# Kernel optimization log

Measured on AMD Instinct MI355X. Metric: run time of the kernel, lower is better.

## Reference

```python
import jax, jax.numpy as jnp
import numpy as np

N_NODES = 100000


def setup_inputs() -> dict:
    key = jax.random.key(0)
    ks = jax.random.split(key, 6)
    x = jax.random.normal(ks[0], (N_NODES, 128), dtype=jnp.float32)
    edge_index = jax.random.randint(ks[1], (2, 1600000), 0, N_NODES, dtype=jnp.int32)
    W_gcn = jax.random.normal(ks[2], (128, 128), dtype=jnp.float32) * 0.05
    b_gcn = jax.random.normal(ks[3], (128,), dtype=jnp.float32) * 0.05
    W_fc = jax.random.normal(ks[4], (64, 128), dtype=jnp.float32) * 0.05
    b_fc = jax.random.normal(ks[5], (64,), dtype=jnp.float32) * 0.05
    return {"x": x, "edge_index": edge_index, "W_gcn": W_gcn, "b_gcn": b_gcn, "W_fc": W_fc, "b_fc": b_fc}


def _gcn_conv(x, edge_index, W, b):
    N = x.shape[0]
    # add self-loops (PyG GCNConv default add_self_loops=True)
    loops = jnp.arange(N, dtype=edge_index.dtype)
    row = jnp.concatenate([edge_index[0], loops])  # source
    col = jnp.concatenate([edge_index[1], loops])  # target (aggregation index)
    # symmetric normalization: deg computed at target with unit edge weights
    deg = jax.ops.segment_sum(jnp.ones_like(col, dtype=x.dtype), col, num_segments=N)
    deg_inv_sqrt = jnp.where(deg > 0, jax.lax.rsqrt(deg), 0.0)
    norm = deg_inv_sqrt[row] * deg_inv_sqrt[col]  # [E+N]
    xw = x @ W  # [N, nhid] - transform before aggregation
    msgs = norm[:, None] * xw[row]  # gather + scale, [E+N, nhid]
    out = jax.ops.segment_sum(msgs, col, num_segments=N)  # scatter-add
    return out + b


def reference(x, edge_index, W_gcn, b_gcn, W_fc, b_fc):
    h = _gcn_conv(x, edge_index, W_gcn, b_gcn)  # [N, nhid]
    return h @ W_fc.T + b_fc  # [N, nclass]
```

## Files before the change

kernel.cpp:

```cpp
#include <hip/hip_runtime.h>
#include <hip/hip_bf16.h>

typedef __hip_bfloat16 bf16;

#define N_NODES 100000
#define N_EDGES 1600000
#define F_IN    128
#define F_OUT   64
#define NBLK    391

#define NB_BKT   196
#define BKT_SH   9
#define BKT_CAP  8960
#define LBIN_CAP 56
#define EPB_A    4096


typedef __attribute__((ext_vector_type(8))) short vbf8;
typedef __attribute__((ext_vector_type(4))) float vf4;

__device__ __forceinline__ float ldf(const void* p, size_t i, bool isbf) {
    return isbf ? __bfloat162float(((const bf16*)p)[i]) : ((const float*)p)[i];
}
__device__ __forceinline__ void stf(void* p, size_t i, bool isbf, float v) {
    if (isbf) ((bf16*)p)[i] = __float2bfloat16(v);
    else      ((float*)p)[i] = v;
}
__device__ __forceinline__ unsigned short f2bfu(float f) {
    __hip_bfloat16 h = __float2bfloat16(f);
    union { __hip_bfloat16 h; unsigned short u; } c; c.h = h; return c.u;
}
__device__ __forceinline__ float bflo(unsigned int u) { return __uint_as_float(u << 16); }
__device__ __forceinline__ float bfhi(unsigned int u) { return __uint_as_float(u & 0xffff0000u); }

__device__ __forceinline__ void splitbf(float f, short& h, short& l) {
    unsigned short hu = f2bfu(f);
    float hf = bflo((unsigned)hu << 0 ? (unsigned)hu << 16 >> 16 << 16 : 0u);
    (void)hf;
    h = (short)hu;
    l = (short)f2bfu(f - __uint_as_float((unsigned)hu << 16));
}

__global__ void k_detect(const unsigned short* __restrict__ w, int* __restrict__ flag) {
    int l = threadIdx.x;
    int good = 0;
#pragma unroll
    for (int q = 0; q < 2; ++q) {
        unsigned short v = w[2 * (l + 64 * q)];
        int e = (v >> 7) & 0xFF;
        if ((e >= 100 && e <= 140) || ((v & 0x7FFF) == 0)) good++;
    }
    unsigned long long m1 = __ballot(good >= 1), m2 = __ballot(good >= 2);
    if (l == 0) *flag = (__popcll(m1) + __popcll(m2) >= 96) ? 1 : 0;
}

__global__ void k_weights(const int* __restrict__ flag,
                          const void* __restrict__ Wg, const void* __restrict__ bg,
                          const void* __restrict__ Wf, const void* __restrict__ bfc,
                          float* __restrict__ M, float* __restrict__ cvec,
                          bf16* __restrict__ Mhi, bf16* __restrict__ Mlo) {
    bool isbf = (*flag != 0);
    int t = blockIdx.x * blockDim.x + threadIdx.x;
    if (t >= F_IN * F_OUT) return;
    int k = t >> 6, c = t & 63;
    float s = 0.f;
    for (int j = 0; j < F_IN; ++j)
        s += ldf(Wg, k * F_IN + j, isbf) * ldf(Wf, c * F_IN + j, isbf);
    M[k * F_OUT + c] = s;
    if (Mhi) {
        int l    = (((k >> 3) & 3) << 4) | (c & 15);
        int fidx = ((((k >> 5) << 2) + (c >> 4)) * 64 + l) * 8 + (k & 7);
        bf16 h  = __float2bfloat16(s);
        Mhi[fidx] = h;
        Mlo[fidx] = __float2bfloat16(s - __bfloat162float(h));
    }
    if (k == 0) {
        float cs = ldf(bfc, c, isbf);
        for (int j = 0; j < F_IN; ++j)
            cs += ldf(bg, j, isbf) * ldf(Wf, c * F_IN + j, isbf);
        cvec[c] = cs;
    }
}


__global__ void k_zero(int* __restrict__ gtail) {
    int i = threadIdx.x;
    if (i < NB_BKT) gtail[i] = 0;
}

__global__ __launch_bounds__(256) void k_binA(const int* __restrict__ ei,
                                              int* __restrict__ gtail,
                                              unsigned* __restrict__ bkt) {
    __shared__ unsigned lbin[NB_BKT * LBIN_CAP];
    __shared__ int lcnt[NB_BKT];
    __shared__ int lbase[NB_BKT];
    int t = threadIdx.x;
    for (int b = t; b < NB_BKT; b += 256) lcnt[b] = 0;
    __syncthreads();
    int e0 = blockIdx.x * EPB_A;
#pragma unroll
    for (int q = 0; q < EPB_A / 256; ++q) {
        int e = e0 + q * 256 + t;
        if (e < N_EDGES) {
            int r = ei[e], c = ei[N_EDGES + e];
            int b = c >> BKT_SH;
            unsigned val = (unsigned)r | ((unsigned)(c & ((1 << BKT_SH) - 1)) << 17);
            int p = atomicAdd(&lcnt[b], 1);
            if (p < LBIN_CAP) {
                lbin[b * LBIN_CAP + p] = val;
            } else {
                int gp = atomicAdd(&gtail[b], 1);
                if (gp < BKT_CAP) bkt[(size_t)b * BKT_CAP + gp] = val;
            }
        }
    }
    __syncthreads();
    for (int b = t; b < NB_BKT; b += 256) {
        int n = min(lcnt[b], LBIN_CAP);
        lbase[b] = atomicAdd(&gtail[b], n);
    }
    __syncthreads();
    int w = t >> 6, l = t & 63;
    for (int b = w; b < NB_BKT; b += 4) {
        int nB = min(lcnt[b], LBIN_CAP);
        int gp0 = lbase[b];
        for (int i = l; i < nB; i += 64) {
            int gp = gp0 + i;
            if (gp < BKT_CAP) bkt[(size_t)b * BKT_CAP + gp] = lbin[b * LBIN_CAP + i];
        }
    }
}

__global__ void k_bktscan(const int* __restrict__ gtail, int* __restrict__ bbase) {
    __shared__ int sm[256];
    int t = threadIdx.x;
    int v = (t < NB_BKT) ? min(gtail[t], BKT_CAP) : 0;
    sm[t] = v; __syncthreads();
    for (int s = 1; s < 256; s <<= 1) {
        int add = (t >= s) ? sm[t - s] : 0;
        __syncthreads();
        sm[t] += add;
        __syncthreads();
    }
    if (t < NB_BKT) bbase[t] = sm[t] - v;
}

__global__ __launch_bounds__(512) void k_build(const unsigned* __restrict__ bkt,
                                               const int* __restrict__ gtail,
                                               const int* __restrict__ bbase,
                                               int* __restrict__ ptr,
                                               int* __restrict__ cnt,
                                               float* __restrict__ dinv,
                                               int* __restrict__ srcs) {
    __shared__ int cntl[512], sm[512], fill[512];
    int b = blockIdx.x, t = threadIdx.x;
    int n = min(gtail[b], BKT_CAP);
    int base = bbase[b];
    cntl[t] = 0;
    __syncthreads();
    for (int i = t; i < n; i += 512)
        atomicAdd(&cntl[bkt[(size_t)b * BKT_CAP + i] >> 17], 1);
    __syncthreads();
    int v = cntl[t];
    sm[t] = v; __syncthreads();
    for (int s = 1; s < 512; s <<= 1) {
        int add = (t >= s) ? sm[t - s] : 0;
        __syncthreads();
        sm[t] += add;
        __syncthreads();
    }
    int excl = sm[t] - v;
    fill[t] = excl;
    int node = (b << BKT_SH) + t;
    if (node < N_NODES) {
        ptr[node]  = base + excl;
        cnt[node]  = v;
        dinv[node] = rsqrtf((float)(v + 1));
    }
    __syncthreads();
    for (int i = t; i < n; i += 512) {
        unsigned e = bkt[(size_t)b * BKT_CAP + i];
        int c = (int)(e >> 17);
        int p = atomicAdd(&fill[c], 1);
        srcs[base + p] = (int)(e & 0x1FFFF);
    }
}

__global__ __launch_bounds__(256) void k_xmz_mfma(const int* __restrict__ flag,
                                                  const void* __restrict__ x,
                                                  const bf16* __restrict__ Mhi,
                                                  const bf16* __restrict__ Mlo,
                                                  const float* __restrict__ dinv,
                                                  bf16* __restrict__ y) {
    int t = threadIdx.x;
    int w = t >> 6, lane = t & 63;
    int g = lane >> 4, cb = lane & 15;
    int r0 = blockIdx.x * 64 + w * 16;
    int rr = min(r0 + cb, N_NODES - 1);
    bool isbf = (*flag != 0);
    const vbf8* Bh = (const vbf8*)Mhi;
    const vbf8* Bl = (const vbf8*)Mlo;
    vf4 acc0 = {0.f,0.f,0.f,0.f}, acc1 = {0.f,0.f,0.f,0.f};
    vf4 acc2 = {0.f,0.f,0.f,0.f}, acc3 = {0.f,0.f,0.f,0.f};

    if (isbf) {
        const vbf8* X8 = (const vbf8*)x;
#pragma unroll
        for (int kk = 0; kk < 4; ++kk) {
            vbf8 a = X8[(size_t)rr * 16 + kk * 4 + g];
            int bb = kk * 256 + lane;
            acc0 = __builtin_amdgcn_mfma_f32_16x16x32_bf16(a, Bh[bb      ], acc0, 0, 0, 0);
            acc0 = __builtin_amdgcn_mfma_f32_16x16x32_bf16(a, Bl[bb      ], acc0, 0, 0, 0);
            acc1 = __builtin_amdgcn_mfma_f32_16x16x32_bf16(a, Bh[bb +  64], acc1, 0, 0, 0);
            acc1 = __builtin_amdgcn_mfma_f32_16x16x32_bf16(a, Bl[bb +  64], acc1, 0, 0, 0);
            acc2 = __builtin_amdgcn_mfma_f32_16x16x32_bf16(a, Bh[bb + 128], acc2, 0, 0, 0);
            acc2 = __builtin_amdgcn_mfma_f32_16x16x32_bf16(a, Bl[bb + 128], acc2, 0, 0, 0);
            acc3 = __builtin_amdgcn_mfma_f32_16x16x32_bf16(a, Bh[bb + 192], acc3, 0, 0, 0);
            acc3 = __builtin_amdgcn_mfma_f32_16x16x32_bf16(a, Bl[bb + 192], acc3, 0, 0, 0);
        }
    } else {
        const float4* X4 = (const float4*)x;
#pragma unroll
        for (int kk = 0; kk < 4; ++kk) {
            float4 v0 = X4[(size_t)rr * 32 + kk * 8 + g * 2];
            float4 v1 = X4[(size_t)rr * 32 + kk * 8 + g * 2 + 1];
            vbf8 ah, al;
            {
                float fv[8] = {v0.x, v0.y, v0.z, v0.w, v1.x, v1.y, v1.z, v1.w};
#pragma unroll
                for (int i = 0; i < 8; ++i) {
                    unsigned short hu = f2bfu(fv[i]);
                    ah[i] = (short)hu;
                    al[i] = (short)f2bfu(fv[i] - __uint_as_float((unsigned)hu << 16));
                }
            }
            int bb = kk * 256 + lane;
            vbf8 b0h = Bh[bb      ], b0l = Bl[bb      ];
            vbf8 b1h = Bh[bb +  64], b1l = Bl[bb +  64];
            vbf8 b2h = Bh[bb + 128], b2l = Bl[bb + 128];
            vbf8 b3h = Bh[bb + 192], b3l = Bl[bb + 192];
            acc0 = __builtin_amdgcn_mfma_f32_16x16x32_bf16(ah, b0h, acc0, 0, 0, 0);
            acc0 = __builtin_amdgcn_mfma_f32_16x16x32_bf16(ah, b0l, acc0, 0, 0, 0);
            acc0 = __builtin_amdgcn_mfma_f32_16x16x32_bf16(al, b0h, acc0, 0, 0, 0);
            acc1 = __builtin_amdgcn_mfma_f32_16x16x32_bf16(ah, b1h, acc1, 0, 0, 0);
            acc1 = __builtin_amdgcn_mfma_f32_16x16x32_bf16(ah, b1l, acc1, 0, 0, 0);
            acc1 = __builtin_amdgcn_mfma_f32_16x16x32_bf16(al, b1h, acc1, 0, 0, 0);
            acc2 = __builtin_amdgcn_mfma_f32_16x16x32_bf16(ah, b2h, acc2, 0, 0, 0);
            acc2 = __builtin_amdgcn_mfma_f32_16x16x32_bf16(ah, b2l, acc2, 0, 0, 0);
            acc2 = __builtin_amdgcn_mfma_f32_16x16x32_bf16(al, b2h, acc2, 0, 0, 0);
            acc3 = __builtin_amdgcn_mfma_f32_16x16x32_bf16(ah, b3h, acc3, 0, 0, 0);
            acc3 = __builtin_amdgcn_mfma_f32_16x16x32_bf16(ah, b3l, acc3, 0, 0, 0);
            acc3 = __builtin_amdgcn_mfma_f32_16x16x32_bf16(al, b3h, acc3, 0, 0, 0);
        }
    }

    unsigned short* yb = (unsigned short*)y;
#pragma unroll
    for (int i = 0; i < 4; ++i) {
        int r = r0 + g * 4 + i;
        if (r < N_NODES) {
            float d = dinv[r];
            unsigned short* yr = yb + (size_t)r * F_OUT + cb;
            yr[0]  = f2bfu(acc0[i] * d);
            yr[16] = f2bfu(acc1[i] * d);
            yr[32] = f2bfu(acc2[i] * d);
            yr[48] = f2bfu(acc3[i] * d);
        }
    }
}

__global__ __launch_bounds__(256) void k_agg(const int* __restrict__ flag,
                                             const int* __restrict__ ptr,
                                             const int* __restrict__ cnt,
                                             const int* __restrict__ srcs,
                                             const float* __restrict__ dinv,
                                             const bf16* __restrict__ y,
                                             const float* __restrict__ cvec,
                                             void* __restrict__ out) {
    int wid  = (blockIdx.x * 256 + threadIdx.x) >> 6;
    int lane = threadIdx.x & 63;
    int g  = lane >> 3;
    int j8 = lane & 7;
    int node = wid * 8 + g;
    bool alive = node < N_NODES;
    int n = 0, start = 0;
    if (alive) { n = cnt[node]; start = ptr[node]; }
    const uint4* y4 = (const uint4*)y;

    float acc[8];
#pragma unroll
    for (int i = 0; i < 8; ++i) acc[i] = 0.f;

    for (int b = 0; __any(b < n); b += 8) {
        int s = 0;
        int idx = b + j8;
        if (idx < n) s = srcs[start + idx];
#pragma unroll
        for (int k = 0; k < 8; ++k) {
            int su = __shfl(s, (g << 3) | k, 64);
            if (b + k < n) {
                uint4 v = y4[(size_t)su * 8 + j8];
                acc[0] += bflo(v.x); acc[1] += bfhi(v.x);
                acc[2] += bflo(v.y); acc[3] += bfhi(v.y);
                acc[4] += bflo(v.z); acc[5] += bfhi(v.z);
                acc[6] += bflo(v.w); acc[7] += bfhi(v.w);
            }
        }
    }

    if (!alive) return;
    bool isbf = (*flag != 0);
    uint4 sv = y4[(size_t)node * 8 + j8];
    float dn = dinv[node];
    const float4* cv4 = (const float4*)cvec;
    float4 c0 = cv4[j8 * 2], c1 = cv4[j8 * 2 + 1];
    size_t ob = (size_t)node * F_OUT + j8 * 8;
    if (isbf) {
        ushort4 p0, p1;
        p0.x = f2bfu(dn * (acc[0] + bflo(sv.x)) + c0.x);
        p0.y = f2bfu(dn * (acc[1] + bfhi(sv.x)) + c0.y);
        p0.z = f2bfu(dn * (acc[2] + bflo(sv.y)) + c0.z);
        p0.w = f2bfu(dn * (acc[3] + bfhi(sv.y)) + c0.w);
        p1.x = f2bfu(dn * (acc[4] + bflo(sv.z)) + c1.x);
        p1.y = f2bfu(dn * (acc[5] + bfhi(sv.z)) + c1.y);
        p1.z = f2bfu(dn * (acc[6] + bflo(sv.w)) + c1.z);
        p1.w = f2bfu(dn * (acc[7] + bfhi(sv.w)) + c1.w);
        ushort4* ob4 = (ushort4*)((unsigned short*)out + ob);
        ob4[0] = p0; ob4[1] = p1;
    } else {
        float4 q0, q1;
        q0.x = dn * (acc[0] + bflo(sv.x)) + c0.x;
        q0.y = dn * (acc[1] + bfhi(sv.x)) + c0.y;
        q0.z = dn * (acc[2] + bflo(sv.y)) + c0.z;
        q0.w = dn * (acc[3] + bfhi(sv.y)) + c0.w;
        q1.x = dn * (acc[4] + bflo(sv.z)) + c1.x;
        q1.y = dn * (acc[5] + bfhi(sv.z)) + c1.y;
        q1.z = dn * (acc[6] + bflo(sv.w)) + c1.z;
        q1.w = dn * (acc[7] + bfhi(sv.w)) + c1.w;
        float4* of4 = (float4*)((float*)out + ob);
        of4[0] = q0; of4[1] = q1;
    }
}


__global__ void k_init_deg(float* __restrict__ deg) {
    int i = blockIdx.x * blockDim.x + threadIdx.x;
    if (i < N_NODES) deg[i] = 1.0f;
}
__global__ void k_deg(const int* __restrict__ col, float* __restrict__ deg) {
    int e = blockIdx.x * blockDim.x + threadIdx.x;
    if (e < N_EDGES) atomicAdd(&deg[col[e]], 1.0f);
}
__global__ void k_dinv(float* __restrict__ deg) {
    int i = blockIdx.x * blockDim.x + threadIdx.x;
    if (i < N_NODES) deg[i] = rsqrtf(deg[i]);
}
__global__ __launch_bounds__(256) void k_xm(const int* __restrict__ flag,
                                            const void* __restrict__ x,
                                            const float* __restrict__ M,
                                            void* __restrict__ z) {
    __shared__ float Ms[F_IN * F_OUT];
    int t = threadIdx.x;
    for (int i = t; i < F_IN * F_OUT; i += 256) Ms[i] = M[i];
    __syncthreads();
    bool isbf = (*flag != 0);
    int r = blockIdx.x * 4 + (t >> 6);
    int c = t & 63;
    if (r >= N_NODES) return;
    float s = 0.f;
    if (isbf) {
        const bf16* xr = (const bf16*)x + (size_t)r * F_IN;
#pragma unroll
        for (int k = 0; k < F_IN; ++k) s += __bfloat162float(xr[k]) * Ms[k * F_OUT + c];
    } else {
        const float* xr = (const float*)x + (size_t)r * F_IN;
#pragma unroll
        for (int k = 0; k < F_IN; ++k) s += xr[k] * Ms[k * F_OUT + c];
    }
    stf(z, (size_t)r * F_OUT + c, isbf, s);
}
template <int LOGF>
__global__ __launch_bounds__(256) void k_init_acc(const int* __restrict__ flag,
                                                  const float* __restrict__ dinv,
                                                  const void* __restrict__ z,
                                                  float* __restrict__ acc, int base) {
    bool isbf = (*flag != 0);
    int t = blockIdx.x * 256 + threadIdx.x;
    int i = t >> LOGF, f = t & ((1 << LOGF) - 1);
    if (i >= N_NODES) return;
    float d = dinv[i];
    acc[t] = d * d * ldf(z, (size_t)i * F_OUT + base + f, isbf);
}
template <int LOGF>
__global__ __launch_bounds__(256) void k_scatter(const int* __restrict__ flag,
                                                 const int* __restrict__ ei,
                                                 const float* __restrict__ dinv,
                                                 const void* __restrict__ z,
                                                 float* __restrict__ acc, int base) {
    bool isbf = (*flag != 0);
    long long t = (long long)blockIdx.x * 256 + threadIdx.x;
    int e = (int)(t >> LOGF), f = (int)(t & ((1 << LOGF) - 1));
    if (e >= N_EDGES) return;
    int r = ei[e], c = ei[N_EDGES + e];
    float nm = dinv[r] * dinv[c];
    float v  = nm * ldf(z, (size_t)r * F_OUT + base + f, isbf);
    atomicAdd(&acc[((size_t)c << LOGF) + f], v);
}
template <int LOGF>
__global__ __launch_bounds__(256) void k_final(const int* __restrict__ flag,
                                               const float* __restrict__ acc,
                                               const float* __restrict__ cvec,
                                               void* __restrict__ out, int base) {
    bool isbf = (*flag != 0);
    int t = blockIdx.x * 256 + threadIdx.x;
    int i = t >> LOGF, f = t & ((1 << LOGF) - 1);
    if (i >= N_NODES) return;
    stf(out, (size_t)i * F_OUT + base + f, isbf, acc[t] + cvec[base + f]);
}
template <int LOGF>
static void run_passes(const int* flag, const int* ei, const float* dinv,
                       const void* z, float* acc, const float* cvec, void* out,
                       hipStream_t stream) {
    const int fpp = 1 << LOGF;
    const long long tn = (long long)N_NODES * fpp;
    const long long te = (long long)N_EDGES * fpp;
    const int gn = (int)((tn + 255) / 256);
    const int ge = (int)((te + 255) / 256);
    for (int base = 0; base < F_OUT; base += fpp) {
        k_init_acc<LOGF><<<gn, 256, 0, stream>>>(flag, dinv, z, acc, base);
        k_scatter<LOGF><<<ge, 256, 0, stream>>>(flag, ei, dinv, z, acc, base);
        k_final<LOGF><<<gn, 256, 0, stream>>>(flag, acc, cvec, out, base);
    }
}

extern "C" void kernel_launch(void* const* d_in, const int* in_sizes, int n_in,
                              void* d_out, int out_size, void* d_ws, size_t ws_size,
                              hipStream_t stream) {
    const void* x   = d_in[0];
    const int*  ei  = (const int*)d_in[1];
    const void* Wg  = d_in[2];
    const void* bg  = d_in[3];
    const void* Wf  = d_in[4];
    const void* bfc = d_in[5];
    char* ws = (char*)d_ws;

    const size_t CSR_NEED = 20871168;
    if (ws_size >= CSR_NEED) {
        int*      flag  = (int*)(ws + 0);
        float*    dinv  = (float*)(ws + 256);
        float*    M     = (float*)(ws + 400384);
        float*    cvec  = (float*)(ws + 433152);
        int*      cnt   = (int*)(ws + 433664);
        int*      ptr   = (int*)(ws + 833664);
        int*      gtail = (int*)(ws + 1233664);
        int*      bbase = (int*)(ws + 1234560);
        int*      srcs  = (int*)(ws + 1238528);
        bf16*     y     = (bf16*)(ws + 8038400);
        unsigned* bkt   = (unsigned*)(ws + 8038400);
        bf16*     Mhi   = (bf16*)(ws + 20838400);
        bf16*     Mlo   = (bf16*)(ws + 20854784);

        k_detect<<<1, 64, 0, stream>>>((const unsigned short*)x, flag);
        k_zero<<<1, 256, 0, stream>>>(gtail);
        k_weights<<<(F_IN * F_OUT) / 256, 256, 0, stream>>>(flag, Wg, bg, Wf, bfc, M, cvec, Mhi, Mlo);
        k_binA<<<(N_EDGES + EPB_A - 1) / EPB_A, 256, 0, stream>>>(ei, gtail, bkt);
        k_bktscan<<<1, 256, 0, stream>>>(gtail, bbase);
        k_build<<<NB_BKT, 512, 0, stream>>>(bkt, gtail, bbase, ptr, cnt, dinv, srcs);
        k_xmz_mfma<<<(N_NODES + 63) / 64, 256, 0, stream>>>(flag, x, Mhi, Mlo, dinv, y);
        k_agg<<<3125, 256, 0, stream>>>(flag, ptr, cnt, srcs, dinv, y, cvec, d_out);
    } else {
        int*   flag = (int*)(ws + 0);
        float* deg  = (float*)(ws + 256);
        float* M    = (float*)(ws + 400384);
        float* cvec = (float*)(ws + 433152);
        float* acc  = (float*)(ws + 433664);

        k_detect<<<1, 64, 0, stream>>>((const unsigned short*)x, flag);
        k_init_deg<<<NBLK, 256, 0, stream>>>(deg);
        k_deg<<<N_EDGES / 256, 256, 0, stream>>>(ei + N_EDGES, deg);
        k_dinv<<<NBLK, 256, 0, stream>>>(deg);
        k_weights<<<(F_IN * F_OUT) / 256, 256, 0, stream>>>(flag, Wg, bg, Wf, bfc, M, cvec, (bf16*)nullptr, (bf16*)nullptr);
        k_xm<<<N_NODES / 4, 256, 0, stream>>>(flag, x, M, d_out);
        const size_t bn = 433664;
        if      (ws_size >= bn + (400000ull << 6)) run_passes<6>(flag, ei, deg, d_out, acc, cvec, d_out, stream);
        else if (ws_size >= bn + (400000ull << 5)) run_passes<5>(flag, ei, deg, d_out, acc, cvec, d_out, stream);
        else if (ws_size >= bn + (400000ull << 4)) run_passes<4>(flag, ei, deg, d_out, acc, cvec, d_out, stream);
        else if (ws_size >= bn + (400000ull << 3)) run_passes<3>(flag, ei, deg, d_out, acc, cvec, d_out, stream);
        else if (ws_size >= bn + (400000ull << 2)) run_passes<2>(flag, ei, deg, d_out, acc, cvec, d_out, stream);
        else if (ws_size >= bn + (400000ull << 1)) run_passes<1>(flag, ei, deg, d_out, acc, cvec, d_out, stream);
        else                                       run_passes<0>(flag, ei, deg, d_out, acc, cvec, d_out, stream);
    }
}
```

Baseline: 222.1 us.

## Use finer CSR buckets, vectorize edge loads, fold gtail zeroing into detect

Bucket count doubles to 391 with 256 nodes per bucket. This gives the CSR build kernel twice as many blocks, each half as large, so more of the GPU's CUs stay busy. The binning kernel now reads edge indices as int4 vectors, and the separate gtail-zeroing kernel is merged into the detect kernel to save one launch. The per-block LDS bins get smaller, so more edges overflow to global atomics. The bucket capacity now leaves less slack for uneven in-degree.

Result: slower. 227.4 us (+2.4%).

```diff
diff --git a/kernel.cpp b/kernel.cpp
--- a/kernel.cpp
+++ b/kernel.cpp
@@ -9,10 +9,10 @@
 #define F_OUT   64
 #define NBLK    391
 
-#define NB_BKT   196
-#define BKT_SH   9
-#define BKT_CAP  8960
-#define LBIN_CAP 56
+#define NB_BKT   391
+#define BKT_SH   8
+#define BKT_CAP  4544
+#define LBIN_CAP 32
 #define EPB_A    4096
 
 
@@ -33,25 +33,23 @@
 __device__ __forceinline__ float bflo(unsigned int u) { return __uint_as_float(u << 16); }
 __device__ __forceinline__ float bfhi(unsigned int u) { return __uint_as_float(u & 0xffff0000u); }
 
-__device__ __forceinline__ void splitbf(float f, short& h, short& l) {
-    unsigned short hu = f2bfu(f);
-    float hf = bflo((unsigned)hu << 0 ? (unsigned)hu << 16 >> 16 << 16 : 0u);
-    (void)hf;
-    h = (short)hu;
-    l = (short)f2bfu(f - __uint_as_float((unsigned)hu << 16));
-}
-
-__global__ void k_detect(const unsigned short* __restrict__ w, int* __restrict__ flag) {
-    int l = threadIdx.x;
-    int good = 0;
-#pragma unroll
-    for (int q = 0; q < 2; ++q) {
-        unsigned short v = w[2 * (l + 64 * q)];
-        int e = (v >> 7) & 0xFF;
-        if ((e >= 100 && e <= 140) || ((v & 0x7FFF) == 0)) good++;
-    }
-    unsigned long long m1 = __ballot(good >= 1), m2 = __ballot(good >= 2);
-    if (l == 0) *flag = (__popcll(m1) + __popcll(m2) >= 96) ? 1 : 0;
+__global__ void k_detect(const unsigned short* __restrict__ w, int* __restrict__ flag,
+                         int* __restrict__ gtail) {
+    int t = threadIdx.x;
+    if (gtail) {
+        for (int i = t; i < NB_BKT; i += 512) gtail[i] = 0;
+    }
+    if (t < 64) {
+        int good = 0;
+#pragma unroll
+        for (int q = 0; q < 2; ++q) {
+            unsigned short v = w[2 * (t + 64 * q)];
+            int e = (v >> 7) & 0xFF;
+            if ((e >= 100 && e <= 140) || ((v & 0x7FFF) == 0)) good++;
+        }
+        unsigned long long m1 = __ballot(good >= 1), m2 = __ballot(good >= 2);
+        if (t == 0) *flag = (__popcll(m1) + __popcll(m2) >= 96) ? 1 : 0;
+    }
 }
 
 __global__ void k_weights(const int* __restrict__ flag,
@@ -83,11 +81,6 @@
 }
 
 
-__global__ void k_zero(int* __restrict__ gtail) {
-    int i = threadIdx.x;
-    if (i < NB_BKT) gtail[i] = 0;
-}
-
 __global__ __launch_bounds__(256) void k_binA(const int* __restrict__ ei,
                                               int* __restrict__ gtail,
                                               unsigned* __restrict__ bkt) {
@@ -97,20 +90,27 @@
     int t = threadIdx.x;
     for (int b = t; b < NB_BKT; b += 256) lcnt[b] = 0;
     __syncthreads();
-    int e0 = blockIdx.x * EPB_A;
-#pragma unroll
-    for (int q = 0; q < EPB_A / 256; ++q) {
-        int e = e0 + q * 256 + t;
-        if (e < N_EDGES) {
-            int r = ei[e], c = ei[N_EDGES + e];
-            int b = c >> BKT_SH;
-            unsigned val = (unsigned)r | ((unsigned)(c & ((1 << BKT_SH) - 1)) << 17);
-            int p = atomicAdd(&lcnt[b], 1);
-            if (p < LBIN_CAP) {
-                lbin[b * LBIN_CAP + p] = val;
-            } else {
-                int gp = atomicAdd(&gtail[b], 1);
-                if (gp < BKT_CAP) bkt[(size_t)b * BKT_CAP + gp] = val;
+    int v0 = blockIdx.x * (EPB_A / 4);
+#pragma unroll
+    for (int q = 0; q < 4; ++q) {
+        int vi = v0 + q * 256 + t;
+        if (vi * 4 < N_EDGES) {
+            int4 rv = ((const int4*)ei)[vi];
+            int4 cv = ((const int4*)(ei + N_EDGES))[vi];
+            int rs[4] = {rv.x, rv.y, rv.z, rv.w};
+            int cs[4] = {cv.x, cv.y, cv.z, cv.w};
+#pragma unroll
+            for (int j = 0; j < 4; ++j) {
+                int r = rs[j], c = cs[j];
+                int b = c >> BKT_SH;
+                unsigned val = (unsigned)r | ((unsigned)(c & ((1 << BKT_SH) - 1)) << 17);
+                int p = atomicAdd(&lcnt[b], 1);
+                if (p < LBIN_CAP) {
+                    lbin[b * LBIN_CAP + p] = val;
+                } else {
+                    int gp = atomicAdd(&gtail[b], 1);
+                    if (gp < BKT_CAP) bkt[(size_t)b * BKT_CAP + gp] = val;
+                }
             }
         }
     }
@@ -132,11 +132,11 @@
 }
 
 __global__ void k_bktscan(const int* __restrict__ gtail, int* __restrict__ bbase) {
-    __shared__ int sm[256];
+    __shared__ int sm[512];
     int t = threadIdx.x;
     int v = (t < NB_BKT) ? min(gtail[t], BKT_CAP) : 0;
     sm[t] = v; __syncthreads();
-    for (int s = 1; s < 256; s <<= 1) {
+    for (int s = 1; s < 512; s <<= 1) {
         int add = (t >= s) ? sm[t - s] : 0;
         __syncthreads();
         sm[t] += add;
@@ -145,25 +145,25 @@
     if (t < NB_BKT) bbase[t] = sm[t] - v;
 }
 
-__global__ __launch_bounds__(512) void k_build(const unsigned* __restrict__ bkt,
+__global__ __launch_bounds__(256) void k_build(const unsigned* __restrict__ bkt,
                                                const int* __restrict__ gtail,
                                                const int* __restrict__ bbase,
                                                int* __restrict__ ptr,
                                                int* __restrict__ cnt,
                                                float* __restrict__ dinv,
                                                int* __restrict__ srcs) {
-    __shared__ int cntl[512], sm[512], fill[512];
+    __shared__ int cntl[256], sm[256], fill[256];
     int b = blockIdx.x, t = threadIdx.x;
     int n = min(gtail[b], BKT_CAP);
     int base = bbase[b];
     cntl[t] = 0;
     __syncthreads();
-    for (int i = t; i < n; i += 512)
+    for (int i = t; i < n; i += 256)
         atomicAdd(&cntl[bkt[(size_t)b * BKT_CAP + i] >> 17], 1);
     __syncthreads();
     int v = cntl[t];
     sm[t] = v; __syncthreads();
-    for (int s = 1; s < 512; s <<= 1) {
+    for (int s = 1; s < 256; s <<= 1) {
         int add = (t >= s) ? sm[t - s] : 0;
         __syncthreads();
         sm[t] += add;
@@ -178,7 +178,7 @@
         dinv[node] = rsqrtf((float)(v + 1));
     }
     __syncthreads();
-    for (int i = t; i < n; i += 512) {
+    for (int i = t; i < n; i += 256) {
         unsigned e = bkt[(size_t)b * BKT_CAP + i];
         int c = (int)(e >> 17);
         int p = atomicAdd(&fill[c], 1);
@@ -453,19 +453,18 @@
         int*      cnt   = (int*)(ws + 433664);
         int*      ptr   = (int*)(ws + 833664);
         int*      gtail = (int*)(ws + 1233664);
-        int*      bbase = (int*)(ws + 1234560);
+        int*      bbase = (int*)(ws + 1235264);
         int*      srcs  = (int*)(ws + 1238528);
         bf16*     y     = (bf16*)(ws + 8038400);
         unsigned* bkt   = (unsigned*)(ws + 8038400);
         bf16*     Mhi   = (bf16*)(ws + 20838400);
         bf16*     Mlo   = (bf16*)(ws + 20854784);
 
-        k_detect<<<1, 64, 0, stream>>>((const unsigned short*)x, flag);
-        k_zero<<<1, 256, 0, stream>>>(gtail);
+        k_detect<<<1, 512, 0, stream>>>((const unsigned short*)x, flag, gtail);
         k_weights<<<(F_IN * F_OUT) / 256, 256, 0, stream>>>(flag, Wg, bg, Wf, bfc, M, cvec, Mhi, Mlo);
         k_binA<<<(N_EDGES + EPB_A - 1) / EPB_A, 256, 0, stream>>>(ei, gtail, bkt);
-        k_bktscan<<<1, 256, 0, stream>>>(gtail, bbase);
-        k_build<<<NB_BKT, 512, 0, stream>>>(bkt, gtail, bbase, ptr, cnt, dinv, srcs);
+        k_bktscan<<<1, 512, 0, stream>>>(gtail, bbase);
+        k_build<<<NB_BKT, 256, 0, stream>>>(bkt, gtail, bbase, ptr, cnt, dinv, srcs);
         k_xmz_mfma<<<(N_NODES + 63) / 64, 256, 0, stream>>>(flag, x, Mhi, Mlo, dinv, y);
         k_agg<<<3125, 256, 0, stream>>>(flag, ptr, cnt, srcs, dinv, y, cvec, d_out);
     } else {
@@ -475,7 +474,7 @@
         float* cvec = (float*)(ws + 433152);
         float* acc  = (float*)(ws + 433664);
 
-        k_detect<<<1, 64, 0, stream>>>((const unsigned short*)x, flag);
+        k_detect<<<1, 512, 0, stream>>>((const unsigned short*)x, flag, (int*)nullptr);
         k_init_deg<<<NBLK, 256, 0, stream>>>(deg);
         k_deg<<<N_EDGES / 256, 256, 0, stream>>>(ei + N_EDGES, deg);
         k_dinv<<<NBLK, 256, 0, stream>>>(deg);
```
